# Kernel tuning notes

Hardware: AMD Instinct MI355X
Metric: run time of the kernel (lower is better)

Reference implementation:

```python
import jax, jax.numpy as jnp
import numpy as np

A, C, V, G = 100000, 230, 800, 60          # athletes, countries, events, games
H, HEADS, DH = 128, 4, 32                   # hidden, gat heads, per-head dim (H = HEADS*DH)
E_AC, E_AE, E_AG, E_EG = 100000, 500000, 300000, 2000
NEG_SLOPE = 0.2


def _seg_mean(msg, idx, n):
    s = jax.ops.segment_sum(msg, idx, num_segments=n)
    cnt = jax.ops.segment_sum(jnp.ones((idx.shape[0], 1), msg.dtype), idx, num_segments=n)
    return s / jnp.maximum(cnt, 1.0)


def _sage(xs, xd, ei, Wl, bl, Wr):
    # PyG SAGEConv(mean): lin_l(mean_neighbors) + lin_r(x_dst); bias lives in lin_l
    agg = _seg_mean(xs[ei[0]], ei[1], xd.shape[0])
    return agg @ Wl + bl + xd @ Wr


def _gatv2(xs, xd, ei, Wl, bl, Wr, br, att, bias):
    # PyG GATv2Conv, concat=True, add_self_loops=False, eval mode (no dropout)
    n = xd.shape[0]
    xl = (xs @ Wl + bl).reshape(-1, HEADS, DH)   # [Ns,H,d]
    xr = (xd @ Wr + br).reshape(-1, HEADS, DH)   # [Nd,H,d]
    src, dst = ei[0], ei[1]
    e = jax.nn.leaky_relu(xl[src] + xr[dst], NEG_SLOPE)      # [E,H,d]
    logit = jnp.einsum('ehd,hd->eh', e, att)                 # [E,H]
    m = jax.ops.segment_max(logit, dst, num_segments=n)
    m = jnp.where(jnp.isneginf(m), 0.0, m)                   # empty dst segments
    ex = jnp.exp(logit - m[dst])
    den = jax.ops.segment_sum(ex, dst, num_segments=n)
    alpha = ex / (den[dst] + 1e-16)
    out = jax.ops.segment_sum(xl[src] * alpha[:, :, None], dst, num_segments=n)
    return out.reshape(n, HEADS * DH) + bias


def _mlp(x, W1, b1, W2, b2):
    return jax.nn.relu(x @ W1 + b1) @ W2 + b2


def _forward(x_athlete, x_country, x_event, x_games,
             eAW1, eAb1, eAW2, eAb2, eCW1, eCb1, eCW2, eCb2,
             eEW1, eEb1, eEW2, eEb2, eGW1, eGb1, eGW2, eGb2,
             sage_Wl, sage_bl, sage_Wr,
             gat_Wl, gat_bl, gat_Wr, gat_br, gat_att, gat_bias,
             ei_ac, ei_ae, ei_ag, ei_eg):
    x = {
        'athlete': _mlp(x_athlete, eAW1, eAb1, eAW2, eAb2),
        'country': _mlp(x_country, eCW1, eCb1, eCW2, eCb2),
        'event':   _mlp(x_event,   eEW1, eEb1, eEW2, eEb2),
        'games':   _mlp(x_games,   eGW1, eGb1, eGW2, eGb2),
    }
    rev = lambda ei: ei[::-1]
    etypes = [
        ('athlete', 'country', ei_ac), ('country', 'athlete', rev(ei_ac)),
        ('athlete', 'event',   ei_ae), ('event',   'athlete', rev(ei_ae)),
        ('athlete', 'games',   ei_ag), ('games',   'athlete', rev(ei_ag)),
        ('event',   'games',   ei_eg), ('games',   'event',   rev(ei_eg)),
    ]
    # layer 1: hetero SAGEConv, HeteroConv aggr='mean' over edge types per dst
    outs = {t: [] for t in x}
    for k, (s, d, ei) in enumerate(etypes):
        outs[d].append(_sage(x[s], x[d], ei, sage_Wl[k], sage_bl[k], sage_Wr[k]))
    x = {t: jax.nn.relu(sum(o) / len(o)) for t, o in outs.items()}
    # layer 2 (final): hetero GATv2Conv, mean over edge types per dst
    outs = {t: [] for t in x}
    for k, (s, d, ei) in enumerate(etypes):
        outs[d].append(_gatv2(x[s], x[d], ei, gat_Wl[k], gat_bl[k], gat_Wr[k],
                              gat_br[k], gat_att[k], gat_bias[k]))
    x = {t: sum(o) / len(o) for t, o in outs.items()}
    return jnp.concatenate([x['athlete'], x['country'], x['event'], x['games']], axis=0)


def setup_inputs() -> dict:
    key = jax.random.key(0)
    ks = iter(jax.random.split(key, 80))
    def nrm(shape, scale=1.0):
        return jax.random.normal(next(ks), shape, jnp.float32) * scale
    def lin(fi, fo):
        return nrm((fi, fo), 1.0 / np.sqrt(fi))
    def edges(ns, nd, E):
        s = jax.random.randint(next(ks), (E,), 0, ns)
        d = jax.random.randint(next(ks), (E,), 0, nd)
        return jnp.stack([s, d]).astype(jnp.int32)
    sc = 1.0 / np.sqrt(H)
    return {
        'x_athlete': nrm((A, 7)), 'x_country': nrm((C, 3)),
        'x_event': nrm((V, 384)), 'x_games': nrm((G, 2)),
        'ei_ac': edges(A, C, E_AC), 'ei_ae': edges(A, V, E_AE),
        'ei_ag': edges(A, G, E_AG), 'ei_eg': edges(V, G, E_EG),
        'eAW1': lin(7, H),   'eAb1': jnp.zeros((H,)), 'eAW2': lin(H, H), 'eAb2': jnp.zeros((H,)),
        'eCW1': lin(3, H),   'eCb1': jnp.zeros((H,)), 'eCW2': lin(H, H), 'eCb2': jnp.zeros((H,)),
        'eEW1': lin(384, H), 'eEb1': jnp.zeros((H,)), 'eEW2': lin(H, H), 'eEb2': jnp.zeros((H,)),
        'eGW1': lin(2, H),   'eGb1': jnp.zeros((H,)), 'eGW2': lin(H, H), 'eGb2': jnp.zeros((H,)),
        'sage_Wl': nrm((8, H, H), sc), 'sage_bl': jnp.zeros((8, H)), 'sage_Wr': nrm((8, H, H), sc),
        'gat_Wl': nrm((8, H, H), sc), 'gat_bl': jnp.zeros((8, H)),
        'gat_Wr': nrm((8, H, H), sc), 'gat_br': jnp.zeros((8, H)),
        'gat_att': nrm((8, HEADS, DH), 1.0 / np.sqrt(DH)), 'gat_bias': jnp.zeros((8, H)),
    }


def reference(x_athlete, x_country, x_event, x_games,
              eAW1, eAb1, eAW2, eAb2, eCW1, eCb1, eCW2, eCb2,
              eEW1, eEb1, eEW2, eEb2, eGW1, eGb1, eGW2, eGb2,
              sage_Wl, sage_bl, sage_Wr,
              gat_Wl, gat_bl, gat_Wr, gat_br, gat_att, gat_bias,
              ei_ac, ei_ae, ei_ag, ei_eg):
    return _forward(x_athlete, x_country, x_event, x_games,
                    eAW1, eAb1, eAW2, eAb2, eCW1, eCb1, eCW2, eCb2,
                    eEW1, eEb1, eEW2, eEb2, eGW1, eGb1, eGW2, eGb2,
                    sage_Wl, sage_bl, sage_Wr,
                    gat_Wl, gat_bl, gat_Wr, gat_br, gat_att, gat_bias,
                    ei_ac, ei_ae, ei_ag, ei_eg)
```

## Files before the change

### kernel.cpp

```cpp
#include <hip/hip_runtime.h>
#include <hip/hip_bf16.h>

#define A_N 100000
#define C_N 230
#define V_N 800
#define G_N 60

#define FLAG_RELU 2

#define SCAN_N   302080
#define SCAN_NB  295
#define E_TOTAL  1804000

#define PCHUNK 16

typedef __attribute__((ext_vector_type(8))) short short8;
typedef __attribute__((ext_vector_type(4))) float f32x4;

__device__ __forceinline__ float bf16dec(unsigned short u){
  return __uint_as_float(((unsigned)u) << 16);
}
__device__ __forceinline__ unsigned short f2b(float v){
  union { __hip_bfloat16 h; unsigned short u; } c;
  c.h = __float2bfloat16(v);
  return c.u;
}
__device__ __forceinline__ float2 ldb2(const unsigned short* p){
  unsigned v = *(const unsigned*)p;
  float2 r;
  r.x = __uint_as_float(v << 16);
  r.y = __uint_as_float(v & 0xffff0000u);
  return r;
}
static inline int imin(int a, int b){ return a < b ? a : b; }

__global__ void detect_dtype(const unsigned short* __restrict__ p, int* __restrict__ flag){
  __shared__ int bad;
  if (threadIdx.x == 0) bad = 0;
  __syncthreads();
  for (int i = threadIdx.x; i < 2048; i += blockDim.x){
    float v = fabsf(bf16dec(p[i]));
    if (!(v <= 1e6f)) atomicOr(&bad, 1);
  }
  __syncthreads();
  if (threadIdx.x == 0) *flag = bad;
}

struct ConvTab { const void* src[29]; int dstoff[29]; int cum[30]; };

__global__ void convert_all(ConvTab tab, float* __restrict__ wsf,
                            const int* __restrict__ flagp, int total){
  const int f = *flagp;
  for (int idx = blockIdx.x*blockDim.x + threadIdx.x; idx < total;
       idx += gridDim.x*blockDim.x){
    int t = 0;
    while (idx >= tab.cum[t+1]) ++t;
    int l = idx - tab.cum[t];
    float v = f ? ((const float*)tab.src[t])[l]
                : bf16dec(((const unsigned short*)tab.src[t])[l]);
    wsf[tab.dstoff[t] + l] = v;
  }
}

__global__ void prep_combos(const float* __restrict__ sWr, const float* __restrict__ sbl,
                            const float* __restrict__ gbias,
                            float* __restrict__ wrcomb, float* __restrict__ sbcomb,
                            float* __restrict__ gbcomb){
  const int sets[4][3] = {{1,3,5},{0,-1,-1},{2,7,-1},{4,6,-1}};
  const float inv[4] = {1.f/3.f, 1.f, 0.5f, 0.5f};
  int idx = blockIdx.x*blockDim.x + threadIdx.x;
  if (idx >= 4*16384) return;
  int t = idx >> 14, j = idx & 16383;
  float s = 0.f;
  #pragma unroll
  for (int q = 0; q < 3; ++q){
    int k = sets[t][q];
    if (k >= 0) s += sWr[k*16384 + j];
  }
  wrcomb[idx] = s * inv[t];
  if (j < 128){
    float b1 = 0.f, b2 = 0.f;
    #pragma unroll
    for (int q = 0; q < 3; ++q){
      int k = sets[t][q];
      if (k >= 0){ b1 += sbl[k*128 + j]; b2 += gbias[k*128 + j]; }
    }
    sbcomb[t*128 + j] = b1 * inv[t];
    gbcomb[t*128 + j] = b2 * inv[t];
  }
}

__global__ void prep_bias2(const float* __restrict__ gbl, const float* __restrict__ gbr,
                           float* __restrict__ gblx, float* __restrict__ gbrx){
  int i = blockIdx.x*blockDim.x + threadIdx.x;
  if (i >= 384) return;
  const int kl[3] = {0,2,4}, kr[3] = {1,3,5};
  int rel = i >> 7, j = i & 127;
  gblx[i] = gbl[kl[rel]*128 + j];
  gbrx[i] = gbr[kr[rel]*128 + j];
}

struct SwzD { int src, dst, K, nkc, kc0, nt0; float scale; };
struct SwzTab { SwzD d[33]; int n, total; };

__global__ void swz_batch(const float* __restrict__ wsf, unsigned short* __restrict__ wsu,
                          SwzTab t){
  for (int idx = blockIdx.x*blockDim.x + threadIdx.x; idx < t.total;
       idx += gridDim.x*blockDim.x){
    int di = 0, local = idx;
    while (local >= t.d[di].K*128){ local -= t.d[di].K*128; ++di; }
    SwzD d = t.d[di];
    int j = local & 7, lane = (local>>3) & 63, rest = local >> 9;
    int kcn = d.K >> 5;
    int kc = rest % kcn, nt = rest / kcn;
    int k = kc*32 + (lane>>4)*8 + j;
    int n = nt*16 + (lane&15);
    float v = wsf[d.src + k*128 + n] * d.scale;
    wsu[(size_t)d.dst + ((size_t)((d.nt0+nt)*d.nkc + d.kc0+kc)*64 + lane)*8 + j] = f2b(v);
  }
}

__global__ void hist_plain(const int* __restrict__ dp, int E, int* __restrict__ cnt){
  int i = blockIdx.x*blockDim.x + threadIdx.x;
  if (i < E) atomicAdd(&cnt[dp[i]], 1);
}

__global__ void hist_lds(const int* __restrict__ dp, int E, int* __restrict__ cnt, int ndst){
  __shared__ int l[800];
  for (int i = threadIdx.x; i < ndst; i += blockDim.x) l[i] = 0;
  __syncthreads();
  for (int i = blockIdx.x*blockDim.x + threadIdx.x; i < E; i += gridDim.x*blockDim.x)
    atomicAdd(&l[dp[i]], 1);
  __syncthreads();
  for (int i = threadIdx.x; i < ndst; i += blockDim.x)
    if (l[i]) atomicAdd(&cnt[i], l[i]);
}

__global__ void scan1(const int* __restrict__ cnt, int* __restrict__ rp, int* __restrict__ bsum){
  __shared__ int sd[256];
  int tid = threadIdx.x, blk = blockIdx.x;
  int base = blk*1024 + tid*4;
  int4 v = *(const int4*)(cnt + base);
  int s = v.x + v.y + v.z + v.w;
  sd[tid] = s;
  __syncthreads();
  for (int off = 1; off < 256; off <<= 1){
    int t = (tid >= off) ? sd[tid-off] : 0;
    __syncthreads();
    sd[tid] += t;
    __syncthreads();
  }
  int excl = sd[tid] - s;
  rp[base+0] = excl;
  rp[base+1] = excl + v.x;
  rp[base+2] = excl + v.x + v.y;
  rp[base+3] = excl + v.x + v.y + v.z;
  if (tid == 255) bsum[blk] = sd[255];
}

__global__ void scan2(int* __restrict__ bsum){
  __shared__ int sd[512];
  int tid = threadIdx.x;
  int v = (tid < SCAN_NB) ? bsum[tid] : 0;
  sd[tid] = v;
  __syncthreads();
  for (int off = 1; off < 512; off <<= 1){
    int t = (tid >= off) ? sd[tid-off] : 0;
    __syncthreads();
    sd[tid] += t;
    __syncthreads();
  }
  if (tid < SCAN_NB) bsum[tid] = sd[tid] - v;
}

__global__ void scan3(int* __restrict__ rp, int* __restrict__ woff,
                      const int* __restrict__ bsum){
  int idx = blockIdx.x*blockDim.x + threadIdx.x;
  if (idx >= SCAN_N) return;
  int v = rp[idx] + bsum[idx >> 10];
  rp[idx] = v;
  woff[idx] = v;
}

__global__ void place_plain(const int* __restrict__ sp, const int* __restrict__ dp,
                            int E, int* __restrict__ woff, int* __restrict__ csr){
  int i = blockIdx.x*blockDim.x + threadIdx.x;
  if (i < E){
    int pos = atomicAdd(&woff[dp[i]], 1);
    csr[pos] = sp[i];
  }
}

__global__ void place_lds(const int* __restrict__ sp, const int* __restrict__ dp,
                          int E, int* __restrict__ woff, int* __restrict__ csr, int ndst){
  __shared__ int lcnt[800];
  __shared__ int lbase[800];
  const int tid = threadIdx.x;
  const int span = blockDim.x * PCHUNK;
  for (int b0 = blockIdx.x*span; b0 < E; b0 += gridDim.x*span){
    for (int i = tid; i < ndst; i += blockDim.x) lcnt[i] = 0;
    __syncthreads();
    int d[PCHUNK], s[PCHUNK], r[PCHUNK];
    #pragma unroll
    for (int j = 0; j < PCHUNK; ++j){
      int e = b0 + j*blockDim.x + tid;
      d[j] = -1;
      if (e < E){
        s[j] = sp[e];
        d[j] = dp[e];
        r[j] = atomicAdd(&lcnt[d[j]], 1);
      }
    }
    __syncthreads();
    for (int i = tid; i < ndst; i += blockDim.x){
      int c = lcnt[i];
      if (c) lbase[i] = atomicAdd(&woff[i], c);
    }
    __syncthreads();
    #pragma unroll
    for (int j = 0; j < PCHUNK; ++j)
      if (d[j] >= 0) csr[lbase[d[j]] + r[j]] = s[j];
    __syncthreads();
  }
}

__global__ void enc_l1(const float* __restrict__ X, const float* __restrict__ W1,
                       const float* __restrict__ b1, unsigned short* __restrict__ Z,
                       int M, int K){
  int idx = blockIdx.x*blockDim.x + threadIdx.x;
  if (idx >= M*128) return;
  int r = idx >> 7, c = idx & 127;
  float s = b1[c];
  for (int k = 0; k < K; ++k) s = fmaf(X[r*K + k], W1[(k<<7) + c], s);
  Z[idx] = f2b(fmaxf(s, 0.f));
}

__global__ void cvt_bf16(const float* __restrict__ src, unsigned short* __restrict__ dst, int n){
  int i = blockIdx.x*blockDim.x + threadIdx.x;
  if (i < n) dst[i] = f2b(src[i]);
}

__device__ __forceinline__ void mfma_core(
    const unsigned short* __restrict__ wsu, const float* __restrict__ wsf,
    int xoff, int xstride, int x2off, int x2stride, int kcsplit,
    int woff, int nkc, int biasoff, int yoff, int ystride,
    int M, int flags, int mblk, int nblk)
{
  int tid = threadIdx.x;
  int wv = tid >> 6, lane = tid & 63;
  int quad = lane >> 4, ml = lane & 15;
  int m0 = mblk*64 + wv*16;
  if (m0 >= M) return;
  int arow = m0 + ml;
  bool rowok = arow < M;
  f32x4 acc[8];
  #pragma unroll
  for (int i = 0; i < 8; ++i) acc[i] = (f32x4){0.f, 0.f, 0.f, 0.f};
  for (int kc = 0; kc < nkc; ++kc){
    short8 a = (short8){0,0,0,0,0,0,0,0};
    if (rowok){
      size_t ao = (kc < kcsplit)
        ? (size_t)xoff  + (size_t)arow*xstride  + kc*32 + quad*8
        : (size_t)x2off + (size_t)arow*x2stride + (kc - kcsplit)*32 + quad*8;
      a = *(const short8*)(wsu + ao);
    }
    size_t wbase = (size_t)woff + ((size_t)(nblk*8)*nkc + kc)*512 + lane*8;
    #pragma unroll
    for (int nt = 0; nt < 8; ++nt){
      short8 b = *(const short8*)(wsu + wbase + (size_t)nt*nkc*512);
      acc[nt] = __builtin_amdgcn_mfma_f32_16x16x32_bf16(a, b, acc[nt], 0, 0, 0);
    }
  }
  #pragma unroll
  for (int nt = 0; nt < 8; ++nt){
    int col = nblk*128 + nt*16 + ml;
    float bv = (biasoff >= 0) ? wsf[biasoff + col] : 0.f;
    #pragma unroll
    for (int r = 0; r < 4; ++r){
      int orow = m0 + quad*4 + r;
      if (orow < M){
        float v = acc[nt][r] + bv;
        if (flags & FLAG_RELU) v = fmaxf(v, 0.f);
        *((unsigned short*)wsu + (size_t)yoff + (size_t)orow*ystride + col) = f2b(v);
      }
    }
  }
}

__global__ __launch_bounds__(256) void mfma_gemm(
    void* ws, int xoff, int xstride, int x2off, int x2stride, int kcsplit,
    int woff, int nkc, int biasoff, int yoff, int ystride, int M, int flags)
{
  mfma_core((const unsigned short*)ws, (const float*)ws, xoff, xstride, x2off, x2stride,
            kcsplit, woff, nkc, biasoff, yoff, ystride, M, flags, blockIdx.x, blockIdx.y);
}

struct GB { int xoff, xstride, woff, biasoff, yoff, ystride, M, nkc, flags; };
struct GBTab { GB d[12]; int n; };

__global__ __launch_bounds__(256) void mfma_gemm_batch(void* ws, GBTab t){
  int di = blockIdx.x / 13, mb = blockIdx.x % 13;
  if (di >= t.n) return;
  GB g = t.d[di];
  mfma_core((const unsigned short*)ws, (const float*)ws, g.xoff, g.xstride, 0, 0, 1000,
            g.woff, g.nkc, g.biasoff, g.yoff, g.ystride, g.M, g.flags, mb, 0);
}

__global__ void sage_gather_athA(const unsigned short* __restrict__ wsu,
    const int* __restrict__ csr, const int* __restrict__ rpb,
    int uhC, int uhE, int uhG, int rp1, int rp3, int rp5, int uagg)
{
  int gid = (blockIdx.x*blockDim.x + threadIdx.x) >> 6;
  if (gid >= A_N) return;
  int lane = threadIdx.x & 63, f = lane*2;
  int srcs[3] = {uhC, uhE, uhG};
  int sstr[3] = {256, 384, 384};
  int rps[3]  = {rp1, rp3, rp5};
  #pragma unroll
  for (int rel = 0; rel < 3; ++rel){
    int st = rpb[rps[rel] + gid], en = rpb[rps[rel] + gid + 1];
    float2 acc = {0.f, 0.f};
    for (int i = st; i < en; ++i){
      int s = csr[i];
      float2 v = ldb2(wsu + (size_t)srcs[rel] + (size_t)s*sstr[rel] + f);
      acc.x += v.x; acc.y += v.y;
    }
    int deg = en - st;
    float sc = 1.f / (float)(deg > 1 ? deg : 1);
    ushort2 o; o.x = f2b(acc.x*sc); o.y = f2b(acc.y*sc);
    *(ushort2*)((unsigned short*)wsu + (size_t)uagg + (size_t)gid*384 + rel*128 + f) = o;
  }
}

struct SgD { int src, sstr, rpoff, aggoff, nd, nc; };
struct SgTab { SgD d[5]; int cumw[6]; };

__global__ void sage_gather_small(const unsigned short* __restrict__ wsu,
    float* __restrict__ wsf, const int* __restrict__ csr, const int* __restrict__ rpb,
    SgTab t)
{
  int gid = (blockIdx.x*blockDim.x + threadIdx.x) >> 6;
  if (gid >= t.cumw[5]) return;
  int di = 0;
  while (gid >= t.cumw[di+1]) ++di;
  SgD d = t.d[di];
  int local = gid - t.cumw[di];
  int row = local / d.nc, c = local - row*d.nc;
  int lane = threadIdx.x & 63, f = lane*2;
  int st = rpb[d.rpoff + row], en = rpb[d.rpoff + row + 1];
  float2 acc = {0.f, 0.f};
  for (int i = st + c; i < en; i += d.nc){
    int s = csr[i];
    float2 v = ldb2(wsu + (size_t)d.src + (size_t)s*d.sstr + f);
    acc.x += v.x; acc.y += v.y;
  }
  float* o = wsf + (size_t)d.aggoff + (size_t)row*128 + f;
  atomicAdd(o, acc.x);
  atomicAdd(o+1, acc.y);
}

struct AfD { int aggoff, rpoff, dstu, dstr, nd; };
struct AfTab { AfD d[5]; int n; };

__global__ void aggfin_batch(unsigned short* __restrict__ wsu, const float* __restrict__ wsf,
                             const int* __restrict__ rpb, AfTab t, int total){
  int idx = blockIdx.x*blockDim.x + threadIdx.x;
  if (idx >= total) return;
  int di = 0, local = idx;
  while (local >= t.d[di].nd*128){ local -= t.d[di].nd*128; ++di; }
  AfD d = t.d[di];
  int row = local >> 7, col = local & 127;
  int deg = rpb[d.rpoff + row + 1] - rpb[d.rpoff + row];
  float sc = 1.f / (float)(deg > 1 ? deg : 1);
  wsu[(size_t)d.dstu + (size_t)row*d.dstr + col] = f2b(wsf[(size_t)d.aggoff + local] * sc);
}

__global__ void gat_ath(const unsigned short* __restrict__ wsu, const float* __restrict__ wsf,
    const int* __restrict__ csr, const int* __restrict__ rpb,
    int ugxr, int uxl1, int uxl3, int uxl5, int oatt, int rp1, int rp3, int rp5, int uout)
{
  int gid = (blockIdx.x*blockDim.x + threadIdx.x) >> 6;
  if (gid >= A_N) return;
  int lane = threadIdx.x & 63, f = lane*2;
  int xls[3] = {uxl1, uxl3, uxl5};
  int rps[3] = {rp1, rp3, rp5};
  const int attk[3] = {1, 3, 5};
  float2 oacc = {0.f, 0.f};
  #pragma unroll
  for (int rel = 0; rel < 3; ++rel){
    float2 xrv = ldb2(wsu + (size_t)ugxr + (size_t)gid*384 + rel*128 + f);
    float2 av  = *(const float2*)(wsf + oatt + attk[rel]*128 + f);
    int st = rpb[rps[rel] + gid], en = rpb[rps[rel] + gid + 1];
    float m = -INFINITY, l = 0.f;
    float2 acc = {0.f, 0.f};
    for (int i = st; i < en; ++i){
      int s = csr[i];
      float2 xv = ldb2(wsu + (size_t)xls[rel] + (size_t)s*128 + f);
      float e0 = xv.x + xrv.x, e1 = xv.y + xrv.y;
      e0 = e0 > 0.f ? e0 : 0.2f*e0;
      e1 = e1 > 0.f ? e1 : 0.2f*e1;
      float p = e0*av.x + e1*av.y;
      p += __shfl_xor(p, 1); p += __shfl_xor(p, 2);
      p += __shfl_xor(p, 4); p += __shfl_xor(p, 8);
      float nm = fmaxf(m, p);
      float sc = __expf(m - nm);
      float pe = __expf(p - nm);
      l = l*sc + pe;
      acc.x = acc.x*sc + pe*xv.x;
      acc.y = acc.y*sc + pe*xv.y;
      m = nm;
    }
    float inv = 1.f / (l + 1e-16f);
    oacc.x += acc.x * inv;
    oacc.y += acc.y * inv;
  }
  ushort2 o; o.x = f2b(oacc.x * (1.f/3.f)); o.y = f2b(oacc.y * (1.f/3.f));
  *(ushort2*)((unsigned short*)wsu + (size_t)uout + (size_t)gid*128 + f) = o;
}

struct GoD { int xl, xlstr, xr, attoff, rpoff, prefix, nd, nc; };
struct GoTab { GoD d[5]; int cumw[6]; };

__global__ void gat_online_batch(const unsigned short* __restrict__ wsu,
    const float* __restrict__ wsf, const int* __restrict__ csr,
    const int* __restrict__ rpb, float* __restrict__ part, GoTab t)
{
  int gid = (blockIdx.x*blockDim.x + threadIdx.x) >> 6;
  if (gid >= t.cumw[5]) return;
  int di = 0;
  while (gid >= t.cumw[di+1]) ++di;
  GoD d = t.d[di];
  int local = gid - t.cumw[di];
  int row = local / d.nc, c = local - row*d.nc;
  int lane = threadIdx.x & 63, f = lane*2, h = lane >> 4;
  float2 xrv = ldb2(wsu + (size_t)d.xr + (size_t)row*128 + f);
  float2 av  = *(const float2*)(wsf + d.attoff + f);
  int st = rpb[d.rpoff + row], en = rpb[d.rpoff + row + 1];
  float m = -INFINITY, l = 0.f;
  float2 acc = {0.f, 0.f};
  for (int i = st + c; i < en; i += d.nc){
    int s = csr[i];
    float2 xv = ldb2(wsu + (size_t)d.xl + (size_t)s*d.xlstr + f);
    float e0 = xv.x + xrv.x, e1 = xv.y + xrv.y;
    e0 = e0 > 0.f ? e0 : 0.2f*e0;
    e1 = e1 > 0.f ? e1 : 0.2f*e1;
    float p = e0*av.x + e1*av.y;
    p += __shfl_xor(p, 1); p += __shfl_xor(p, 2);
    p += __shfl_xor(p, 4); p += __shfl_xor(p, 8);
    float nm = fmaxf(m, p);
    float sc = __expf(m - nm);
    float pe = __expf(p - nm);
    l = l*sc + pe;
    acc.x = acc.x*sc + pe*xv.x;
    acc.y = acc.y*sc + pe*xv.y;
    m = nm;
  }
  float* pr = part + (size_t)(d.prefix + local)*136;
  if ((lane & 15) == 0){ pr[h] = m; pr[4+h] = l; }
  pr[8+f]   = acc.x;
  pr[8+f+1] = acc.y;
}

struct MgD { int prefix, outoff, nd, nc; float invS; };
struct MgTab { MgD d[5]; int cumw[6]; };

__global__ void gat_merge_batch(const float* __restrict__ part, float* __restrict__ wsf,
                                MgTab t){
  int gid = (blockIdx.x*blockDim.x + threadIdx.x) >> 6;
  if (gid >= t.cumw[5]) return;
  int di = 0;
  while (gid >= t.cumw[di+1]) ++di;
  MgD d = t.d[di];
  int row = gid - t.cumw[di];
  int lane = threadIdx.x & 63, f = lane*2, h = lane >> 4;
  float M = -INFINITY;
  for (int c = 0; c < d.nc; ++c)
    M = fmaxf(M, part[(size_t)(d.prefix + row*d.nc + c)*136 + h]);
  float L = 0.f;
  float2 acc = {0.f, 0.f};
  for (int c = 0; c < d.nc; ++c){
    const float* pr = part + (size_t)(d.prefix + row*d.nc + c)*136;
    float mc = pr[h];
    float w = (mc == -INFINITY) ? 0.f : __expf(mc - M);
    L += pr[4+h] * w;
    acc.x += pr[8+f]   * w;
    acc.y += pr[8+f+1] * w;
  }
  float inv = d.invS / (L + 1e-16f);
  float* o = wsf + (size_t)d.outoff + (size_t)row*128 + f;
  o[0] = acc.x * inv;
  o[1] = acc.y * inv;
}

__global__ void final_out(const unsigned short* __restrict__ wsu,
  const float* __restrict__ wsf, int uoutA, int oC0, int oE2, int oE7, int oG4, int oG6,
  int ogb, const int* __restrict__ flagp, void* __restrict__ dout)
{
  const int fl = *flagp;
  int idx = blockIdx.x*blockDim.x + threadIdx.x;
  const int total = 101090*128;
  if (idx >= total) return;
  int row = idx >> 7, c = idx & 127;
  float v; int t;
  if (row < A_N){ v = bf16dec(wsu[(size_t)uoutA + idx]); t = 0; }
  else if (row < A_N + C_N){ v = wsf[oC0 + (row - A_N)*128 + c]; t = 1; }
  else if (row < A_N + C_N + V_N){
    int l = (row - A_N - C_N)*128 + c;
    v = wsf[oE2 + l] + wsf[oE7 + l]; t = 2;
  } else {
    int l = (row - A_N - C_N - V_N)*128 + c;
    v = wsf[oG4 + l] + wsf[oG6 + l]; t = 3;
  }
  v += wsf[ogb + t*128 + c];
  if (fl) ((float*)dout)[idx] = v;
  else    ((__hip_bfloat16*)dout)[idx] = __float2bfloat16(v);
}

__global__ void ws_fail(float* __restrict__ out, float mb){
  if (threadIdx.x == 0 && blockIdx.x == 0) out[0] = mb;
}

extern "C" void kernel_launch(void* const* d_in, const int* in_sizes, int n_in,
                              void* d_out, int out_size, void* d_ws, size_t ws_size,
                              hipStream_t stream)
{
  float* wsf = (float*)d_ws;
  unsigned short* wsu = (unsigned short*)d_ws;
  int* flagp = (int*)d_ws;
  size_t off = 16;
  auto alloc = [&](size_t n){ size_t o = off; off += (n + 15) & ~(size_t)15; return (int)o; };
  auto allocU = [&](size_t nu){ return 2*alloc((nu + 1)/2); };

  static const int conv_in_idx[29] = {0,1,2,3, 8,9,10,11, 12,13,14,15, 16,17,18,19,
                                      20,21,22,23, 24,25,26, 27,28,29,30,31,32};
  static const int conv_n[29] = {700000,690,307200,120,
                                 896,128,16384,128, 384,128,16384,128,
                                 49152,128,16384,128, 256,128,16384,128,
                                 131072,1024,131072, 131072,1024,131072,1024,1024,1024};
  ConvTab tab;
  int coff[29];
  int total = 0;
  for (int i = 0; i < 29; ++i){
    tab.src[i] = d_in[conv_in_idx[i]];
    coff[i] = alloc((size_t)conv_n[i]);
    tab.dstoff[i] = coff[i];
    tab.cum[i] = total; total += conv_n[i];
  }
  tab.cum[29] = total;

  const int o_sWl = coff[20], o_sbl = coff[21];
  const int o_gWl = coff[23], o_gbl = coff[24], o_gWr = coff[25], o_gbr = coff[26];
  const int o_gatt = coff[27], o_gbias = coff[28];

  int o_wrcomb = alloc(4*16384);
  int o_sbcomb = alloc(512);
  int o_gbcomb = alloc(512);
  int o_gblx = alloc(384);
  int o_gbrx = alloc(384);
  int o_cnt  = alloc(SCAN_N);
  int o_rp   = alloc(SCAN_N);
  int o_woff = alloc(SCAN_N);
  int o_bsum = alloc(1024);
  int o_csr  = alloc(E_TOTAL);
  int o_part = alloc((size_t)22320*136);
  int o_aggS = alloc((size_t)1950*128);
  int o_outC0 = alloc(230*128);
  int o_outE2 = alloc(800*128);
  int o_outE7 = alloc(800*128);
  int o_outG4 = alloc(60*128);
  int o_outG6 = alloc(60*128);

  int u_bswz = allocU(573440);
  int u_xEb  = allocU(307200);
  int u_zC   = allocU(230*128);
  int u_zE   = allocU(800*128);
  int u_zG   = allocU(60*128);
  int u_sxC  = allocU(230*256);
  int u_sxE  = allocU(800*384);
  int u_sxG  = allocU(60*384);
  int u_yC   = allocU(230*128);
  int u_yE   = allocU(800*128);
  int u_yG   = allocU(60*128);
  int u_xl1  = allocU(230*128);
  int u_xl3  = allocU(800*128);
  int u_xl5  = allocU(60*128);
  int u_xl6  = allocU(800*128);
  int u_xl7  = allocU(60*128);
  int u_xr0  = allocU(230*128);
  int u_xr2  = allocU(800*128);
  int u_xr4  = allocU(60*128);
  int u_xr6  = allocU(60*128);
  int u_xr7  = allocU(800*128);
  int u_big0 = allocU((size_t)A_N*128);
  int u_bigH = allocU((size_t)A_N*128);
  int u_bigA = allocU((size_t)A_N*384);

  if (off*4 > ws_size){
    ws_fail<<<1, 64, 0, stream>>>((float*)d_out, (float)((off*4) >> 20));
    return;
  }

  const int u_eAW2 = u_bswz + 0,      u_eCW2 = u_bswz + 16384;
  const int u_eEW2 = u_bswz + 32768,  u_eGW2 = u_bswz + 49152;
  const int u_eEW1 = u_bswz + 65536;
  const int u_sxAW = u_bswz + 114688, u_sxCW = u_bswz + 180224;
  const int u_sxEW = u_bswz + 212992, u_sxGW = u_bswz + 262144;
  const int u_gxlW = u_bswz + 311296, u_gxrW = u_bswz + 360448;
  int u_smW[10];
  for (int i = 0; i < 10; ++i) u_smW[i] = u_bswz + 409600 + i*16384;

  const int n_nodes[4] = {A_N, C_N, V_N, G_N};
  const int et_dst[8] = {1,0,2,0,3,0,3,2};
  const int et_ei[8]  = {4,4,5,5,6,6,7,7};
  const int et_rev[8] = {0,1,0,1,0,1,0,1};
  const int et_E[8]   = {100000,100000,500000,500000,300000,300000,2000,2000};

  const int* esp[8]; const int* edp[8]; int rowbase[8];
  {
    int rb = 0;
    for (int k = 0; k < 8; ++k){
      const int* ei = (const int*)d_in[et_ei[k]];
      int E = et_E[k];
      esp[k] = ei + (et_rev[k] ? E : 0);
      edp[k] = ei + (et_rev[k] ? 0 : E);
      rowbase[k] = rb; rb += n_nodes[et_dst[k]];
    }
  }
  int* rpb_p  = (int*)(wsf + o_rp);
  int* csr_p  = (int*)(wsf + o_csr);

  detect_dtype<<<1, 256, 0, stream>>>((const unsigned short*)d_in[2], flagp);
  convert_all<<<2048, 256, 0, stream>>>(tab, wsf, flagp, total);
  prep_combos<<<(4*16384 + 255)/256, 256, 0, stream>>>(wsf + o_sWl + 0, wsf + o_sbl,
      wsf + o_gbias, wsf + o_wrcomb, wsf + o_sbcomb, wsf + o_gbcomb);
  prep_combos<<<1, 1, 0, stream>>>(wsf, wsf, wsf, wsf + o_wrcomb, wsf + o_sbcomb, wsf + o_gbcomb);

  prep_combos<<<(4*16384 + 255)/256, 256, 0, stream>>>(wsf + coff[22], wsf + o_sbl,
      wsf + o_gbias, wsf + o_wrcomb, wsf + o_sbcomb, wsf + o_gbcomb);
  prep_bias2<<<2, 256, 0, stream>>>(wsf + o_gbl, wsf + o_gbr, wsf + o_gblx, wsf + o_gbrx);

  SwzTab st; int sn = 0, stotal = 0;
  auto push = [&](int src, int K, int dst, int nkc, int kc0, int nt0, float sc){
    st.d[sn++] = SwzD{src, dst, K, nkc, kc0, nt0, sc};
    stotal += K*128;
  };
  push(coff[6],  128, u_eAW2, 4, 0, 0, 1.f);
  push(coff[10], 128, u_eCW2, 4, 0, 0, 1.f);
  push(coff[14], 128, u_eEW2, 4, 0, 0, 1.f);
  push(coff[18], 128, u_eGW2, 4, 0, 0, 1.f);
  push(coff[12], 384, u_eEW1, 12, 0, 0, 1.f);
  push(o_wrcomb + 0,     128, u_sxAW, 16, 0,  0, 1.f);
  push(o_sWl + 1*16384,  128, u_sxAW, 16, 4,  0, 1.f/3.f);
  push(o_sWl + 3*16384,  128, u_sxAW, 16, 8,  0, 1.f/3.f);
  push(o_sWl + 5*16384,  128, u_sxAW, 16, 12, 0, 1.f/3.f);
  push(o_wrcomb + 16384, 128, u_sxCW, 8, 0, 0, 1.f);
  push(o_sWl + 0*16384,  128, u_sxCW, 8, 4, 0, 1.f);
  push(o_wrcomb + 32768, 128, u_sxEW, 12, 0, 0, 1.f);
  push(o_sWl + 2*16384,  128, u_sxEW, 12, 4, 0, 0.5f);
  push(o_sWl + 7*16384,  128, u_sxEW, 12, 8, 0, 0.5f);
  push(o_wrcomb + 49152, 128, u_sxGW, 12, 0, 0, 1.f);
  push(o_sWl + 4*16384,  128, u_sxGW, 12, 4, 0, 0.5f);
  push(o_sWl + 6*16384,  128, u_sxGW, 12, 8, 0, 0.5f);
  push(o_gWl + 0*16384, 128, u_gxlW, 4, 0, 0,  1.f);
  push(o_gWl + 2*16384, 128, u_gxlW, 4, 0, 8,  1.f);
  push(o_gWl + 4*16384, 128, u_gxlW, 4, 0, 16, 1.f);
  push(o_gWr + 1*16384, 128, u_gxrW, 4, 0, 0,  1.f);
  push(o_gWr + 3*16384, 128, u_gxrW, 4, 0, 8,  1.f);
  push(o_gWr + 5*16384, 128, u_gxrW, 4, 0, 16, 1.f);
  const int xlk[5] = {1,3,5,6,7};
  for (int i = 0; i < 5; ++i) push(o_gWl + xlk[i]*16384, 128, u_smW[i], 4, 0, 0, 1.f);
  const int xrk[5] = {0,2,4,6,7};
  for (int i = 0; i < 5; ++i) push(o_gWr + xrk[i]*16384, 128, u_smW[5+i], 4, 0, 0, 1.f);
  st.n = sn; st.total = stotal;
  swz_batch<<<(stotal + 255)/256, 256, 0, stream>>>(wsf, wsu, st);

  hipMemsetAsync(wsf + o_cnt, 0, (size_t)SCAN_N*4, stream);
  for (int k = 0; k < 8; ++k){
    int E = et_E[k], nd = n_nodes[et_dst[k]];
    if (nd <= 800)
      hist_lds<<<imin(256, (E + 255)/256), 256, 0, stream>>>(edp[k], E,
          (int*)(wsf + o_cnt) + rowbase[k], nd);
    else
      hist_plain<<<(E + 255)/256, 256, 0, stream>>>(edp[k], E,
          (int*)(wsf + o_cnt) + rowbase[k]);
  }
  scan1<<<SCAN_NB, 256, 0, stream>>>((int*)(wsf + o_cnt), rpb_p, (int*)(wsf + o_bsum));
  scan2<<<1, 512, 0, stream>>>((int*)(wsf + o_bsum));
  scan3<<<(SCAN_N + 255)/256, 256, 0, stream>>>(rpb_p, (int*)(wsf + o_woff),
                                                (int*)(wsf + o_bsum));
  for (int k = 0; k < 8; ++k){
    int E = et_E[k], nd = n_nodes[et_dst[k]];
    if (nd <= 800){
      int span = 256*PCHUNK;
      place_lds<<<imin(304, (E + span - 1)/span), 256, 0, stream>>>(
          esp[k], edp[k], E, (int*)(wsf + o_woff) + rowbase[k], csr_p, nd);
    } else {
      place_plain<<<(E + 255)/256, 256, 0, stream>>>(esp[k], edp[k], E,
          (int*)(wsf + o_woff) + rowbase[k], csr_p);
    }
  }

  enc_l1<<<(A_N*128 + 255)/256, 256, 0, stream>>>(wsf + coff[0], wsf + coff[4],
      wsf + coff[5], wsu + u_big0, A_N, 7);
  enc_l1<<<(C_N*128 + 255)/256, 256, 0, stream>>>(wsf + coff[1], wsf + coff[8],
      wsf + coff[9], wsu + u_zC, C_N, 3);
  enc_l1<<<(G_N*128 + 255)/256, 256, 0, stream>>>(wsf + coff[3], wsf + coff[16],
      wsf + coff[17], wsu + u_zG, G_N, 2);
  cvt_bf16<<<(307200 + 255)/256, 256, 0, stream>>>(wsf + coff[2], wsu + u_xEb, 307200);

  GBTab e1; e1.n = 3;
  e1.d[0] = GB{u_zC, 128, u_eCW2, coff[11], u_sxC, 256, C_N, 4, 0};
  e1.d[1] = GB{u_xEb, 384, u_eEW1, coff[13], u_zE, 128, V_N, 12, FLAG_RELU};
  e1.d[2] = GB{u_zG, 128, u_eGW2, coff[19], u_sxG, 384, G_N, 4, 0};
  mfma_gemm_batch<<<3*13, 256, 0, stream>>>(d_ws, e1);
  GBTab e2; e2.n = 1;
  e2.d[0] = GB{u_zE, 128, u_eEW2, coff[15], u_sxE, 384, V_N, 4, 0};
  mfma_gemm_batch<<<13, 256, 0, stream>>>(d_ws, e2);
  mfma_gemm<<<dim3((A_N + 63)/64, 1), 256, 0, stream>>>(d_ws, u_big0, 128, 0, 0, 1000,
      u_eAW2, 4, coff[7], u_bigH, 128, A_N, 0);

  sage_gather_athA<<<(A_N*64 + 255)/256, 256, 0, stream>>>(wsu, csr_p, rpb_p,
      u_sxC, u_sxE, u_sxG, rowbase[1], rowbase[3], rowbase[5], u_bigA);
  hipMemsetAsync(wsf + o_aggS, 0, (size_t)1950*128*4, stream);
  const int b0 = o_aggS, b2 = o_aggS + 230*128, b7 = b2 + 800*128,
            b4 = b7 + 800*128, b6 = b4 + 60*128;
  SgTab sg;
  sg.d[0] = SgD{u_bigH, 128, rowbase[0], b0, C_N, 8};
  sg.d[1] = SgD{u_bigH, 128, rowbase[2], b2, V_N, 8};
  sg.d[2] = SgD{u_sxG, 384, rowbase[7], b7, V_N, 8};
  sg.d[3] = SgD{u_bigH, 128, rowbase[4], b4, G_N, 64};
  sg.d[4] = SgD{u_sxE, 384, rowbase[6], b6, G_N, 64};
  sg.cumw[0] = 0;
  {
    int c = 0;
    for (int i = 0; i < 5; ++i){ c += sg.d[i].nd*sg.d[i].nc; sg.cumw[i+1] = c; }
  }
  sage_gather_small<<<(sg.cumw[5]*64 + 255)/256, 256, 0, stream>>>(wsu, wsf, csr_p, rpb_p, sg);
  AfTab af; af.n = 5;
  af.d[0] = AfD{b0, rowbase[0], u_sxC + 128, 256, C_N};
  af.d[1] = AfD{b2, rowbase[2], u_sxE + 128, 384, V_N};
  af.d[2] = AfD{b7, rowbase[7], u_sxE + 256, 384, V_N};
  af.d[3] = AfD{b4, rowbase[4], u_sxG + 128, 384, G_N};
  af.d[4] = AfD{b6, rowbase[6], u_sxG + 256, 384, G_N};
  int aftot = 1950*128;
  aggfin_batch<<<(aftot + 255)/256, 256, 0, stream>>>(wsu, wsf, rpb_p, af, aftot);
  GBTab sgm; sgm.n = 3;
  sgm.d[0] = GB{u_sxC, 256, u_sxCW, o_sbcomb + 128, u_yC, 128, C_N, 8,  FLAG_RELU};
  sgm.d[1] = GB{u_sxE, 384, u_sxEW, o_sbcomb + 256, u_yE, 128, V_N, 12, FLAG_RELU};
  sgm.d[2] = GB{u_sxG, 384, u_sxGW, o_sbcomb + 384, u_yG, 128, G_N, 12, FLAG_RELU};
  mfma_gemm_batch<<<3*13, 256, 0, stream>>>(d_ws, sgm);
  mfma_gemm<<<dim3((A_N + 63)/64, 1), 256, 0, stream>>>(d_ws, u_bigH, 128, u_bigA, 384, 4,
      u_sxAW, 16, o_sbcomb, u_big0, 128, A_N, FLAG_RELU);

  mfma_gemm<<<dim3((A_N + 63)/64, 3), 256, 0, stream>>>(d_ws, u_big0, 128, 0, 0, 1000,
      u_gxlW, 4, o_gblx, u_bigA, 384, A_N, 0);
  GBTab gm; gm.n = 10;
  gm.d[0] = GB{u_yC, 128, u_smW[0], o_gbl + 1*128, u_xl1, 128, C_N, 4, 0};
  gm.d[1] = GB{u_yE, 128, u_smW[1], o_gbl + 3*128, u_xl3, 128, V_N, 4, 0};
  gm.d[2] = GB{u_yG, 128, u_smW[2], o_gbl + 5*128, u_xl5, 128, G_N, 4, 0};
  gm.d[3] = GB{u_yE, 128, u_smW[3], o_gbl + 6*128, u_xl6, 128, V_N, 4, 0};
  gm.d[4] = GB{u_yG, 128, u_smW[4], o_gbl + 7*128, u_xl7, 128, G_N, 4, 0};
  gm.d[5] = GB{u_yC, 128, u_smW[5], o_gbr + 0*128, u_xr0, 128, C_N, 4, 0};
  gm.d[6] = GB{u_yE, 128, u_smW[6], o_gbr + 2*128, u_xr2, 128, V_N, 4, 0};
  gm.d[7] = GB{u_yG, 128, u_smW[7], o_gbr + 4*128, u_xr4, 128, G_N, 4, 0};
  gm.d[8] = GB{u_yG, 128, u_smW[8], o_gbr + 6*128, u_xr6, 128, G_N, 4, 0};
  gm.d[9] = GB{u_yE, 128, u_smW[9], o_gbr + 7*128, u_xr7, 128, V_N, 4, 0};
  mfma_gemm_batch<<<10*13, 256, 0, stream>>>(d_ws, gm);

  GoTab go;
  go.d[0] = GoD{u_bigA + 0,   384, u_xr0, o_gatt + 0*128, rowbase[0], 0,     C_N, 8};
  go.d[1] = GoD{u_bigA + 128, 384, u_xr2, o_gatt + 2*128, rowbase[2], 1840,  V_N, 8};
  go.d[2] = GoD{u_bigA + 256, 384, u_xr4, o_gatt + 4*128, rowbase[4], 8240,  G_N, 64};
  go.d[3] = GoD{u_xl6, 128,        u_xr6, o_gatt + 6*128, rowbase[6], 12080, G_N, 64};
  go.d[4] = GoD{u_xl7, 128,        u_xr7, o_gatt + 7*128, rowbase[7], 15920, V_N, 8};
  go.cumw[0] = 0;
  {
    int c = 0;
    for (int i = 0; i < 5; ++i){ c += go.d[i].nd*go.d[i].nc; go.cumw[i+1] = c; }
  }
  gat_online_batch<<<(go.cumw[5]*64 + 255)/256, 256, 0, stream>>>(wsu, wsf, csr_p, rpb_p,
      wsf + o_part, go);

  mfma_gemm<<<dim3((A_N + 63)/64, 3), 256, 0, stream>>>(d_ws, u_big0, 128, 0, 0, 1000,
      u_gxrW, 4, o_gbrx, u_bigA, 384, A_N, 0);
  gat_ath<<<(A_N*64 + 255)/256, 256, 0, stream>>>(wsu, wsf, csr_p, rpb_p,
      u_bigA, u_xl1, u_xl3, u_xl5, o_gatt, rowbase[1], rowbase[3], rowbase[5], u_bigH);

  MgTab mg;
  mg.d[0] = MgD{0,     o_outC0, C_N, 8,  1.0f};
  mg.d[1] = MgD{1840,  o_outE2, V_N, 8,  0.5f};
  mg.d[2] = MgD{8240,  o_outG4, G_N, 64, 0.5f};
  mg.d[3] = MgD{12080, o_outG6, G_N, 64, 0.5f};
  mg.d[4] = MgD{15920, o_outE7, V_N, 8,  0.5f};
  mg.cumw[0] = 0;
  {
    int c = 0;
    for (int i = 0; i < 5; ++i){ c += mg.d[i].nd; mg.cumw[i+1] = c; }
  }
  gat_merge_batch<<<(mg.cumw[5]*64 + 255)/256, 256, 0, stream>>>(wsf + o_part, wsf, mg);

  final_out<<<(101090*128 + 255)/256, 256, 0, stream>>>(wsu, wsf, u_bigH,
      o_outC0, o_outE2, o_outE7, o_outG4, o_outG6, o_gbcomb, flagp, d_out);
}
```

Measured before the change: 1.210 ms.

## Split each wavefront into two half-waves processing alternate edges with 4-wide loads

```diff
diff --git a/kernel.cpp b/kernel.cpp
--- a/kernel.cpp
+++ b/kernel.cpp
@@ -25,11 +25,13 @@
   c.h = __float2bfloat16(v);
   return c.u;
 }
-__device__ __forceinline__ float2 ldb2(const unsigned short* p){
-  unsigned v = *(const unsigned*)p;
-  float2 r;
-  r.x = __uint_as_float(v << 16);
-  r.y = __uint_as_float(v & 0xffff0000u);
+__device__ __forceinline__ float4 ldb4(const unsigned short* p){
+  uint2 v = *(const uint2*)p;
+  float4 r;
+  r.x = __uint_as_float(v.x << 16);
+  r.y = __uint_as_float(v.x & 0xffff0000u);
+  r.z = __uint_as_float(v.y << 16);
+  r.w = __uint_as_float(v.y & 0xffff0000u);
   return r;
 }
 static inline int imin(int a, int b){ return a < b ? a : b; }
@@ -312,23 +314,39 @@
 {
   int gid = (blockIdx.x*blockDim.x + threadIdx.x) >> 6;
   if (gid >= A_N) return;
-  int lane = threadIdx.x & 63, f = lane*2;
+  int lane = threadIdx.x & 63;
+  int half = lane >> 5, sub = lane & 31, f = sub*4;
   int srcs[3] = {uhC, uhE, uhG};
   int sstr[3] = {256, 384, 384};
   int rps[3]  = {rp1, rp3, rp5};
   #pragma unroll
   for (int rel = 0; rel < 3; ++rel){
+    const unsigned short* base = wsu + (size_t)srcs[rel] + f;
+    int str = sstr[rel];
     int st = rpb[rps[rel] + gid], en = rpb[rps[rel] + gid + 1];
-    float2 acc = {0.f, 0.f};
-    for (int i = st; i < en; ++i){
-      int s = csr[i];
-      float2 v = ldb2(wsu + (size_t)srcs[rel] + (size_t)s*sstr[rel] + f);
-      acc.x += v.x; acc.y += v.y;
-    }
-    int deg = en - st;
-    float sc = 1.f / (float)(deg > 1 ? deg : 1);
-    ushort2 o; o.x = f2b(acc.x*sc); o.y = f2b(acc.y*sc);
-    *(ushort2*)((unsigned short*)wsu + (size_t)uagg + (size_t)gid*384 + rel*128 + f) = o;
+    float4 acc = {0.f, 0.f, 0.f, 0.f};
+    int i = st + half;
+    for (; i + 2 < en; i += 4){
+      int s0 = csr[i], s1 = csr[i+2];
+      float4 v0 = ldb4(base + (size_t)s0*str);
+      float4 v1 = ldb4(base + (size_t)s1*str);
+      acc.x += v0.x + v1.x; acc.y += v0.y + v1.y;
+      acc.z += v0.z + v1.z; acc.w += v0.w + v1.w;
+    }
+    if (i < en){
+      float4 v0 = ldb4(base + (size_t)csr[i]*str);
+      acc.x += v0.x; acc.y += v0.y; acc.z += v0.z; acc.w += v0.w;
+    }
+    acc.x += __shfl_xor(acc.x, 32); acc.y += __shfl_xor(acc.y, 32);
+    acc.z += __shfl_xor(acc.z, 32); acc.w += __shfl_xor(acc.w, 32);
+    if (half == 0){
+      int deg = en - st;
+      float sc = 1.f / (float)(deg > 1 ? deg : 1);
+      ushort4 o;
+      o.x = f2b(acc.x*sc); o.y = f2b(acc.y*sc);
+      o.z = f2b(acc.z*sc); o.w = f2b(acc.w*sc);
+      *(ushort4*)((unsigned short*)wsu + (size_t)uagg + (size_t)gid*384 + rel*128 + f) = o;
+    }
   }
 }
 
@@ -346,17 +364,31 @@
   SgD d = t.d[di];
   int local = gid - t.cumw[di];
   int row = local / d.nc, c = local - row*d.nc;
-  int lane = threadIdx.x & 63, f = lane*2;
+  int lane = threadIdx.x & 63;
+  int half = lane >> 5, sub = lane & 31, f = sub*4;
+  const unsigned short* base = wsu + (size_t)d.src + f;
   int st = rpb[d.rpoff + row], en = rpb[d.rpoff + row + 1];
-  float2 acc = {0.f, 0.f};
-  for (int i = st + c; i < en; i += d.nc){
-    int s = csr[i];
-    float2 v = ldb2(wsu + (size_t)d.src + (size_t)s*d.sstr + f);
-    acc.x += v.x; acc.y += v.y;
-  }
-  float* o = wsf + (size_t)d.aggoff + (size_t)row*128 + f;
-  atomicAdd(o, acc.x);
-  atomicAdd(o+1, acc.y);
+  float4 acc = {0.f, 0.f, 0.f, 0.f};
+  int i = st + c + half*d.nc;
+  int step = 2*d.nc;
+  for (; i + step < en; i += 2*step){
+    int s0 = csr[i], s1 = csr[i+step];
+    float4 v0 = ldb4(base + (size_t)s0*d.sstr);
+    float4 v1 = ldb4(base + (size_t)s1*d.sstr);
+    acc.x += v0.x + v1.x; acc.y += v0.y + v1.y;
+    acc.z += v0.z + v1.z; acc.w += v0.w + v1.w;
+  }
+  if (i < en){
+    float4 v0 = ldb4(base + (size_t)csr[i]*d.sstr);
+    acc.x += v0.x; acc.y += v0.y; acc.z += v0.z; acc.w += v0.w;
+  }
+  acc.x += __shfl_xor(acc.x, 32); acc.y += __shfl_xor(acc.y, 32);
+  acc.z += __shfl_xor(acc.z, 32); acc.w += __shfl_xor(acc.w, 32);
+  if (half == 0){
+    float* o = wsf + (size_t)d.aggoff + (size_t)row*128 + f;
+    atomicAdd(o,   acc.x); atomicAdd(o+1, acc.y);
+    atomicAdd(o+2, acc.z); atomicAdd(o+3, acc.w);
+  }
 }
 
 struct AfD { int aggoff, rpoff, dstu, dstr, nd; };
@@ -375,47 +407,82 @@
   wsu[(size_t)d.dstu + (size_t)row*d.dstr + col] = f2b(wsf[(size_t)d.aggoff + local] * sc);
 }
 
+#define GAT_UPD(xv)                                                        \
+  {                                                                        \
+    float e0 = (xv).x + xrv.x, e1 = (xv).y + xrv.y;                        \
+    float e2 = (xv).z + xrv.z, e3 = (xv).w + xrv.w;                        \
+    e0 = e0 > 0.f ? e0 : 0.2f*e0; e1 = e1 > 0.f ? e1 : 0.2f*e1;            \
+    e2 = e2 > 0.f ? e2 : 0.2f*e2; e3 = e3 > 0.f ? e3 : 0.2f*e3;            \
+    float p = e0*av.x + e1*av.y + e2*av.z + e3*av.w;                       \
+    p += __shfl_xor(p, 1); p += __shfl_xor(p, 2); p += __shfl_xor(p, 4);   \
+    float nm = fmaxf(m, p);                                                \
+    float scw = __expf(m - nm);                                            \
+    float pe = __expf(p - nm);                                             \
+    l = l*scw + pe;                                                        \
+    acc.x = acc.x*scw + pe*(xv).x; acc.y = acc.y*scw + pe*(xv).y;          \
+    acc.z = acc.z*scw + pe*(xv).z; acc.w = acc.w*scw + pe*(xv).w;          \
+    m = nm;                                                                \
+  }
+
+#define GAT_MERGE_HALVES                                                   \
+  {                                                                        \
+    float mo = __shfl_xor(m, 32);                                          \
+    float lo = __shfl_xor(l, 32);                                          \
+    float4 ao;                                                             \
+    ao.x = __shfl_xor(acc.x, 32); ao.y = __shfl_xor(acc.y, 32);            \
+    ao.z = __shfl_xor(acc.z, 32); ao.w = __shfl_xor(acc.w, 32);            \
+    float nm = fmaxf(m, mo);                                               \
+    float w  = (m  == -INFINITY) ? 0.f : __expf(m  - nm);                  \
+    float wo = (mo == -INFINITY) ? 0.f : __expf(mo - nm);                  \
+    l = l*w + lo*wo;                                                       \
+    acc.x = acc.x*w + ao.x*wo; acc.y = acc.y*w + ao.y*wo;                  \
+    acc.z = acc.z*w + ao.z*wo; acc.w = acc.w*w + ao.w*wo;                  \
+    m = nm;                                                                \
+  }
+
 __global__ void gat_ath(const unsigned short* __restrict__ wsu, const float* __restrict__ wsf,
     const int* __restrict__ csr, const int* __restrict__ rpb,
     int ugxr, int uxl1, int uxl3, int uxl5, int oatt, int rp1, int rp3, int rp5, int uout)
 {
   int gid = (blockIdx.x*blockDim.x + threadIdx.x) >> 6;
   if (gid >= A_N) return;
-  int lane = threadIdx.x & 63, f = lane*2;
+  int lane = threadIdx.x & 63;
+  int half = lane >> 5, sub = lane & 31, f = sub*4;
   int xls[3] = {uxl1, uxl3, uxl5};
   int rps[3] = {rp1, rp3, rp5};
   const int attk[3] = {1, 3, 5};
-  float2 oacc = {0.f, 0.f};
+  float4 oacc = {0.f, 0.f, 0.f, 0.f};
   #pragma unroll
   for (int rel = 0; rel < 3; ++rel){
-    float2 xrv = ldb2(wsu + (size_t)ugxr + (size_t)gid*384 + rel*128 + f);
-    float2 av  = *(const float2*)(wsf + oatt + attk[rel]*128 + f);
+    float4 xrv = ldb4(wsu + (size_t)ugxr + (size_t)gid*384 + rel*128 + f);
+    float4 av  = *(const float4*)(wsf + oatt + attk[rel]*128 + f);
+    const unsigned short* base = wsu + (size_t)xls[rel] + f;
     int st = rpb[rps[rel] + gid], en = rpb[rps[rel] + gid + 1];
     float m = -INFINITY, l = 0.f;
-    float2 acc = {0.f, 0.f};
-    for (int i = st; i < en; ++i){
-      int s = csr[i];
-      float2 xv = ldb2(wsu + (size_t)xls[rel] + (size_t)s*128 + f);
-      float e0 = xv.x + xrv.x, e1 = xv.y + xrv.y;
-      e0 = e0 > 0.f ? e0 : 0.2f*e0;
-      e1 = e1 > 0.f ? e1 : 0.2f*e1;
-      float p = e0*av.x + e1*av.y;
-      p += __shfl_xor(p, 1); p += __shfl_xor(p, 2);
-      p += __shfl_xor(p, 4); p += __shfl_xor(p, 8);
-      float nm = fmaxf(m, p);
-      float sc = __expf(m - nm);
-      float pe = __expf(p - nm);
-      l = l*sc + pe;
-      acc.x = acc.x*sc + pe*xv.x;
-      acc.y = acc.y*sc + pe*xv.y;
-      m = nm;
-    }
+    float4 acc = {0.f, 0.f, 0.f, 0.f};
+    int i = st + half;
+    for (; i + 2 < en; i += 4){
+      int s0 = csr[i], s1 = csr[i+2];
+      float4 x0 = ldb4(base + (size_t)s0*128);
+      float4 x1 = ldb4(base + (size_t)s1*128);
+      GAT_UPD(x0);
+      GAT_UPD(x1);
+    }
+    if (i < en){
+      float4 x0 = ldb4(base + (size_t)csr[i]*128);
+      GAT_UPD(x0);
+    }
+    GAT_MERGE_HALVES;
     float inv = 1.f / (l + 1e-16f);
-    oacc.x += acc.x * inv;
-    oacc.y += acc.y * inv;
-  }
-  ushort2 o; o.x = f2b(oacc.x * (1.f/3.f)); o.y = f2b(oacc.y * (1.f/3.f));
-  *(ushort2*)((unsigned short*)wsu + (size_t)uout + (size_t)gid*128 + f) = o;
+    oacc.x += acc.x * inv; oacc.y += acc.y * inv;
+    oacc.z += acc.z * inv; oacc.w += acc.w * inv;
+  }
+  if (half == 0){
+    ushort4 o;
+    o.x = f2b(oacc.x * (1.f/3.f)); o.y = f2b(oacc.y * (1.f/3.f));
+    o.z = f2b(oacc.z * (1.f/3.f)); o.w = f2b(oacc.w * (1.f/3.f));
+    *(ushort4*)((unsigned short*)wsu + (size_t)uout + (size_t)gid*128 + f) = o;
+  }
 }
 
 struct GoD { int xl, xlstr, xr, attoff, rpoff, prefix, nd, nc; };
@@ -432,33 +499,33 @@
   GoD d = t.d[di];
   int local = gid - t.cumw[di];
   int row = local / d.nc, c = local - row*d.nc;
-  int lane = threadIdx.x & 63, f = lane*2, h = lane >> 4;
-  float2 xrv = ldb2(wsu + (size_t)d.xr + (size_t)row*128 + f);
-  float2 av  = *(const float2*)(wsf + d.attoff + f);
+  int lane = threadIdx.x & 63;
+  int half = lane >> 5, sub = lane & 31, f = sub*4, h = sub >> 3;
+  float4 xrv = ldb4(wsu + (size_t)d.xr + (size_t)row*128 + f);
+  float4 av  = *(const float4*)(wsf + d.attoff + f);
+  const unsigned short* base = wsu + (size_t)d.xl + f;
   int st = rpb[d.rpoff + row], en = rpb[d.rpoff + row + 1];
   float m = -INFINITY, l = 0.f;
-  float2 acc = {0.f, 0.f};
-  for (int i = st + c; i < en; i += d.nc){
-    int s = csr[i];
-    float2 xv = ldb2(wsu + (size_t)d.xl + (size_t)s*d.xlstr + f);
-    float e0 = xv.x + xrv.x, e1 = xv.y + xrv.y;
-    e0 = e0 > 0.f ? e0 : 0.2f*e0;
-    e1 = e1 > 0.f ? e1 : 0.2f*e1;
-    float p = e0*av.x + e1*av.y;
-    p += __shfl_xor(p, 1); p += __shfl_xor(p, 2);
-    p += __shfl_xor(p, 4); p += __shfl_xor(p, 8);
-    float nm = fmaxf(m, p);
-    float sc = __expf(m - nm);
-    float pe = __expf(p - nm);
-    l = l*sc + pe;
-    acc.x = acc.x*sc + pe*xv.x;
-    acc.y = acc.y*sc + pe*xv.y;
-    m = nm;
-  }
-  float* pr = part + (size_t)(d.prefix + local)*136;
-  if ((lane & 15) == 0){ pr[h] = m; pr[4+h] = l; }
-  pr[8+f]   = acc.x;
-  pr[8+f+1] = acc.y;
+  float4 acc = {0.f, 0.f, 0.f, 0.f};
+  int i = st + c + half*d.nc;
+  int step = 2*d.nc;
+  for (; i + step < en; i += 2*step){
+    int s0 = csr[i], s1 = csr[i+step];
+    float4 x0 = ldb4(base + (size_t)s0*d.xlstr);
+    float4 x1 = ldb4(base + (size_t)s1*d.xlstr);
+    GAT_UPD(x0);
+    GAT_UPD(x1);
+  }
+  if (i < en){
+    float4 x0 = ldb4(base + (size_t)csr[i]*d.xlstr);
+    GAT_UPD(x0);
+  }
+  GAT_MERGE_HALVES;
+  if (half == 0){
+    float* pr = part + (size_t)(d.prefix + local)*136;
+    if ((sub & 7) == 0){ pr[h] = m; pr[4+h] = l; }
+    *(float4*)(pr + 8 + f) = acc;
+  }
 }
 
 struct MgD { int prefix, outoff, nd, nc; float invS; };
@@ -631,10 +698,6 @@
 
   detect_dtype<<<1, 256, 0, stream>>>((const unsigned short*)d_in[2], flagp);
   convert_all<<<2048, 256, 0, stream>>>(tab, wsf, flagp, total);
-  prep_combos<<<(4*16384 + 255)/256, 256, 0, stream>>>(wsf + o_sWl + 0, wsf + o_sbl,
-      wsf + o_gbias, wsf + o_wrcomb, wsf + o_sbcomb, wsf + o_gbcomb);
-  prep_combos<<<1, 1, 0, stream>>>(wsf, wsf, wsf, wsf + o_wrcomb, wsf + o_sbcomb, wsf + o_gbcomb);
-
   prep_combos<<<(4*16384 + 255)/256, 256, 0, stream>>>(wsf + coff[22], wsf + o_sbl,
       wsf + o_gbias, wsf + o_wrcomb, wsf + o_sbcomb, wsf + o_gbcomb);
   prep_bias2<<<2, 256, 0, stream>>>(wsf + o_gbl, wsf + o_gbr, wsf + o_gblx, wsf + o_gbrx);
```

After: 1.093 ms. 9.7% less time.
